# Performance work log

Hardware: AMD Instinct MI355X
Metric: run time of the kernel (lower is better)

The kernel has to match this reference:

```python
import jax, jax.numpy as jnp
import numpy as np

B, S, H2 = 32, 4096, 512  # H2 = 2*hidden_size


def setup_inputs() -> dict:
    key = jax.random.key(0)
    ks = jax.random.split(key, 10)
    s = 1.0 / np.sqrt(H2)
    return {
        "decoder_state": jax.random.normal(ks[0], (B, 1, H2), jnp.float32),
        "encoder_outputs": jax.random.normal(ks[1], (B, S, H2), jnp.float32),
        "coverage_vector": jax.random.uniform(ks[2], (B, S, H2), jnp.float32),
        "W_h": jax.random.uniform(ks[3], (H2, H2), jnp.float32, -s, s),
        "b_h": jax.random.uniform(ks[4], (H2,), jnp.float32, -s, s),
        "W_s": jax.random.uniform(ks[5], (H2, H2), jnp.float32, -s, s),
        "b_s": jax.random.uniform(ks[6], (H2,), jnp.float32, -s, s),
        "W_c": jax.random.uniform(ks[7], (H2, H2), jnp.float32, -s, s),
        "b_c": jax.random.uniform(ks[8], (H2,), jnp.float32, -s, s),
        "v": jax.random.uniform(ks[9], (H2, 1), jnp.float32, -s, s),
    }


def reference(decoder_state, encoder_outputs, coverage_vector,
              W_h, b_h, W_s, b_s, W_c, b_c, v):
    # additive attention features: [B, S, 2H]
    e = jnp.tanh(encoder_outputs @ W_h + b_h
                 + decoder_state @ W_s + b_s      # broadcasts over S
                 + coverage_vector @ W_c + b_c)
    scores = e @ v                                # [B, S, 1]
    attn_dist = jax.nn.softmax(scores, axis=1)    # softmax over source positions
    # weighted sum of encoder outputs: [B, 1, 2H]
    h_star_t = jnp.einsum('bsi,bsd->bid', attn_dist, encoder_outputs)
    coverage_new = coverage_vector + attn_dist    # broadcast over feature dim
    return h_star_t, attn_dist, coverage_new
```

## Files before the change

### kernel.cpp

```cpp
#include <hip/hip_runtime.h>
#include <hip/hip_bf16.h>
#include <stdint.h>

#define H2    512
#define BATCH 32
#define SEQ   4096
#define BM    64
#define NKT   32

typedef __attribute__((ext_vector_type(4))) float f32x4;
typedef __attribute__((ext_vector_type(8))) short bf16x8;

__device__ __forceinline__ unsigned short f2bf(float f) {
    union { float f; unsigned u; } v; v.f = f;
    unsigned r = v.u + 0x7FFF + ((v.u >> 16) & 1);
    return (unsigned short)(r >> 16);
}

__device__ __forceinline__ uint2 cvt4_bf16(f32x4 a) {
    uint2 r;
    asm("v_cvt_pk_bf16_f32 %0, %1, %2" : "=v"(r.x) : "v"(a[0]), "v"(a[1]));
    asm("v_cvt_pk_bf16_f32 %0, %1, %2" : "=v"(r.y) : "v"(a[2]), "v"(a[3]));
    return r;
}

__device__ __forceinline__ float fast_tanh(float x) {
    float e = __builtin_amdgcn_exp2f(x * 2.88539008177793f);
    return 1.0f - 2.0f * __builtin_amdgcn_rcpf(e + 1.0f);
}

__global__ void kzero(float* __restrict__ p) {
    int i = blockIdx.x * blockDim.x + threadIdx.x;
    if (i < 16416) p[i] = 0.0f;
}

__global__ void kprep_w(const float* __restrict__ Wh, const float* __restrict__ Wc,
                        unsigned short* __restrict__ wt) {
    int c    = blockIdx.x * blockDim.x + threadIdx.x;
    int lane = c & 63;
    int cb   = (c >> 6) & 31;
    int kt   = c >> 11;
    int col  = cb * 16 + (lane & 15);
    int k0   = kt * 32 + (lane >> 4) * 8;
    unsigned short tmp[8];
#pragma unroll
    for (int j = 0; j < 8; ++j) {
        int kg = k0 + j;
        float w = (kg < 512) ? Wh[kg * 512 + col] : Wc[(kg - 512) * 512 + col];
        tmp[j] = f2bf(w);
    }
    *reinterpret_cast<uint4*>(wt + (size_t)c * 8) = *reinterpret_cast<const uint4*>(tmp);
}

__global__ void kprep_q(const float* __restrict__ dec, const float* __restrict__ Ws,
                        const float* __restrict__ bh, const float* __restrict__ bs,
                        const float* __restrict__ bc, float* __restrict__ q) {
    __shared__ float dsh[512];
    int b = blockIdx.x, t = threadIdx.x;
    dsh[t]       = dec[b * 512 + t];
    dsh[t + 256] = dec[b * 512 + 256 + t];
    __syncthreads();
    float a0 = 0.f, a1 = 0.f;
#pragma unroll 4
    for (int k = 0; k < 512; ++k) {
        float d = dsh[k];
        a0 = fmaf(d, Ws[k * 512 + t], a0);
        a1 = fmaf(d, Ws[k * 512 + 256 + t], a1);
    }
    q[b * 512 + t]       = a0 + bh[t] + bs[t] + bc[t];
    q[b * 512 + 256 + t] = a1 + bh[256 + t] + bs[256 + t] + bc[256 + t];
}

__launch_bounds__(512, 4)
__global__ void kgemm(const float* __restrict__ enc, const float* __restrict__ cov,
                      const unsigned short* __restrict__ wt,
                      const float* __restrict__ q, const float* __restrict__ vvec,
                      float* __restrict__ wout, float* __restrict__ hun,
                      float* __restrict__ Zb) {
    __shared__ unsigned short Asm[3][2048];
    __shared__ float qv[H2];
    __shared__ float vv[H2];
    __shared__ float sred[BM][8];
    __shared__ float wsh[BM];

    int tid  = threadIdx.x;
    int lane = tid & 63, wn = tid >> 6;

    int cpx  = gridDim.x >> 3;
    int swz  = (blockIdx.x & 7) * cpx + (blockIdx.x >> 3);
    int row0 = swz * BM;
    int b    = row0 >> 12;

    qv[tid] = q[b * H2 + tid];
    vv[tid] = vvec[tid];

    int r = tid >> 3, k4 = tid & 7;
    const float* aeb = enc + (size_t)(row0 + r) * H2 + k4 * 4;
    const float* acb = cov + (size_t)(row0 + r) * H2 + k4 * 4;
    unsigned awb = (unsigned)((r >> 4) * 1024 + (k4 >> 1) * 256 +
                              (((r & 15) * 16) ^ ((k4 >> 1) << 4)) + (k4 & 1) * 8);
    unsigned arb = (unsigned)((lane >> 4) * 256 +
                              (((lane & 15) * 16) ^ ((lane >> 4) << 4)));
    const bf16x8* bb = reinterpret_cast<const bf16x8*>(wt) +
                       (size_t)(wn * 4) * 64 + lane;

    f32x4  acc[4][4] = {};
    bf16x8 af[4], bfr[4];
    f32x4  pa;

#define A_SRC(T) (((T) < 16) ? (aeb + (T) * 32) : (acb + ((T) - 16) * 32))
#define SB0 __builtin_amdgcn_sched_barrier(0);

    pa = *reinterpret_cast<const f32x4*>(A_SRC(0));
#pragma unroll
    for (int ni = 0; ni < 4; ++ni) bfr[ni] = bb[ni * 64];
    SB0
    { uint2 u = cvt4_bf16(pa);
      *reinterpret_cast<uint2*>((char*)Asm[0] + awb) = u; }
    pa = *reinterpret_cast<const f32x4*>(A_SRC(1));
    SB0
    { uint2 u = cvt4_bf16(pa);
      *reinterpret_cast<uint2*>((char*)Asm[1] + awb) = u; }
    pa = *reinterpret_cast<const f32x4*>(A_SRC(2));
    asm volatile("s_waitcnt lgkmcnt(0)" ::: "memory");
    SB0
    __builtin_amdgcn_s_barrier();
    SB0
#pragma unroll
    for (int mi = 0; mi < 4; ++mi)
        af[mi] = *reinterpret_cast<const bf16x8*>((char*)Asm[0] + mi * 1024 + arb);

    unsigned ro = 4096, wo = 8192;

#pragma unroll 1
    for (int t = 0; t < NKT; ++t) {
        __builtin_amdgcn_s_setprio(1);
#pragma unroll
        for (int mi = 0; mi < 4; ++mi)
#pragma unroll
            for (int ni = 0; ni < 4; ++ni)
                acc[mi][ni] = __builtin_amdgcn_mfma_f32_16x16x32_bf16(
                    af[mi], bfr[ni], acc[mi][ni], 0, 0, 0);
        __builtin_amdgcn_s_setprio(0);
        SB0
        if (t < NKT - 1) {
#pragma unroll
            for (int mi = 0; mi < 4; ++mi)
                af[mi] = *reinterpret_cast<const bf16x8*>(
                    (char*)Asm[0] + ro + mi * 1024 + arb);
            SB0
#pragma unroll
            for (int ni = 0; ni < 4; ++ni)
                bfr[ni] = bb[(size_t)(t + 1) * 2048 + ni * 64];
            SB0
        }
        if (t < NKT - 2) {
            uint2 u = cvt4_bf16(pa);
            *reinterpret_cast<uint2*>((char*)Asm[0] + wo + awb) = u;
        }
        if (t < NKT - 3) {
            pa = *reinterpret_cast<const f32x4*>(A_SRC(t + 3));
        }
        asm volatile("s_waitcnt lgkmcnt(0)" ::: "memory");
        SB0
        __builtin_amdgcn_s_barrier();
        SB0
        ro = (ro == 8192) ? 0u : ro + 4096;
        wo = (wo == 8192) ? 0u : wo + 4096;
    }
#undef A_SRC
#undef SB0

    float ps[4][4] = {};
#pragma unroll
    for (int mi = 0; mi < 4; ++mi)
#pragma unroll
        for (int ni = 0; ni < 4; ++ni) {
            int colg = wn * 64 + ni * 16 + (lane & 15);
            float qq = qv[colg], vl = vv[colg];
#pragma unroll
            for (int j = 0; j < 4; ++j) {
                float e = fast_tanh(acc[mi][ni][j] + qq);
                ps[mi][j] = fmaf(e, vl, ps[mi][j]);
            }
        }
#pragma unroll
    for (int mi = 0; mi < 4; ++mi)
#pragma unroll
        for (int j = 0; j < 4; ++j) {
            float s = ps[mi][j];
            s += __shfl_xor(s, 1);
            s += __shfl_xor(s, 2);
            s += __shfl_xor(s, 4);
            s += __shfl_xor(s, 8);
            if ((lane & 15) == 0)
                sred[mi * 16 + (lane >> 4) * 4 + j][wn] = s;
        }
    __syncthreads();

    if (tid < BM) {
        float s = 0.f;
#pragma unroll
        for (int w = 0; w < 8; ++w) s += sred[tid][w];
        float wv = __builtin_amdgcn_exp2f((s - 16.0f) * 1.4426950408889634f);
        wsh[tid] = wv;
        wout[row0 + tid] = wv;
        float zs = wv;
#pragma unroll
        for (int o = 1; o < 64; o <<= 1) zs += __shfl_xor(zs, o);
        if (tid == 0) atomicAdd(&Zb[b], zs);
    }
    __syncthreads();

    float hacc = 0.f;
#pragma unroll 8
    for (int rr = 0; rr < BM; ++rr)
        hacc = fmaf(wsh[rr], enc[(size_t)(row0 + rr) * H2 + tid], hacc);
    atomicAdd(&hun[b * H2 + tid], hacc);
}

__global__ void knorm(const float* __restrict__ hun, const float* __restrict__ Zb,
                      float* __restrict__ out) {
    int i = blockIdx.x * blockDim.x + threadIdx.x;
    int b = i >> 9;
    out[i] = hun[i] / Zb[b];
}

__global__ void kcov2(const float* __restrict__ cov, const float* __restrict__ w,
                      const float* __restrict__ Zb, float* __restrict__ out) {
    float* attn = out + 16384;
    float* covn = out + 16384 + 131072;
    int blk = blockIdx.x;
    int b = blk >> 6, ck = blk & 63;
    int s0 = ck * 64;
    int t  = threadIdx.x;
    int f4 = (t & 127) * 4;
    int rp = t >> 7;
    float rZ = 1.0f / Zb[b];
    size_t base = (size_t)b * SEQ * H2;
#pragma unroll 2
    for (int i = 0; i < 32; ++i) {
        int s = s0 + i * 2 + rp;
        float a = w[b * 4096 + s] * rZ;
        size_t idx = base + (size_t)s * H2 + f4;
        f32x4 c4 = *reinterpret_cast<const f32x4*>(cov + idx);
        c4 += a;
        __builtin_nontemporal_store(c4, reinterpret_cast<f32x4*>(covn + idx));
        if (f4 == 0) attn[b * 4096 + s] = a;
    }
}

extern "C" void kernel_launch(void* const* d_in, const int* in_sizes, int n_in,
                              void* d_out, int out_size, void* d_ws, size_t ws_size,
                              hipStream_t stream) {
    const float* dec = (const float*)d_in[0];
    const float* enc = (const float*)d_in[1];
    const float* cov = (const float*)d_in[2];
    const float* Wh  = (const float*)d_in[3];
    const float* bh  = (const float*)d_in[4];
    const float* Ws  = (const float*)d_in[5];
    const float* bs  = (const float*)d_in[6];
    const float* Wc  = (const float*)d_in[7];
    const float* bc  = (const float*)d_in[8];
    const float* v   = (const float*)d_in[9];
    float* out = (float*)d_out;

    char* ws = (char*)d_ws;
    unsigned short* wt = (unsigned short*)ws;
    float* q    = (float*)(ws + 0x100000);
    float* wbuf = (float*)(ws + 0x110000);
    float* hun  = (float*)(ws + 0x190000);
    float* Zb   = (float*)(ws + 0x1A0000);

    kzero   <<<dim3(65),   dim3(256),  0, stream>>>(hun);
    kprep_w <<<dim3(256),  dim3(256),  0, stream>>>(Wh, Wc, wt);
    kprep_q <<<dim3(32),   dim3(256),  0, stream>>>(dec, Ws, bh, bs, bc, q);
    kgemm   <<<dim3(2048), dim3(512),  0, stream>>>(enc, cov, wt, q, v,
                                                    wbuf, hun, Zb);
    knorm   <<<dim3(64),   dim3(256),  0, stream>>>(hun, Zb, out);
    kcov2   <<<dim3(2048), dim3(256),  0, stream>>>(cov, wbuf, Zb, out);
}
```

Baseline: 386.0 us.

## Use K=64 double-buffered A staging and replace atomics with partial reductions

The GEMM main loop now stages 64-wide K chunks (8 floats per thread, 16-byte LDS writes) into a two-buffer LDS ring and runs two MFMA groups per barrier, which halves the number of barriers and widens the global loads. Atomic accumulation of the context vector and normaliser is replaced by per-block partial buffers that a reworked knorm kernel reduces, and the zeroing kernel is removed. The weighted-sum loop uses four accumulators. The cost is extra workspace traffic for the partials (about 4MB) and a serial 64-element reduction inside knorm.

```diff
diff --git a/kernel.cpp b/kernel.cpp
--- a/kernel.cpp
+++ b/kernel.cpp
@@ -6,7 +6,7 @@
 #define BATCH 32
 #define SEQ   4096
 #define BM    64
-#define NKT   32
+#define NPER  16
 
 typedef __attribute__((ext_vector_type(4))) float f32x4;
 typedef __attribute__((ext_vector_type(8))) short bf16x8;
@@ -17,21 +17,18 @@
     return (unsigned short)(r >> 16);
 }
 
-__device__ __forceinline__ uint2 cvt4_bf16(f32x4 a) {
-    uint2 r;
-    asm("v_cvt_pk_bf16_f32 %0, %1, %2" : "=v"(r.x) : "v"(a[0]), "v"(a[1]));
-    asm("v_cvt_pk_bf16_f32 %0, %1, %2" : "=v"(r.y) : "v"(a[2]), "v"(a[3]));
+__device__ __forceinline__ uint4 cvt8_bf16(f32x4 lo, f32x4 hi) {
+    uint4 r;
+    asm("v_cvt_pk_bf16_f32 %0, %1, %2" : "=v"(r.x) : "v"(lo[0]), "v"(lo[1]));
+    asm("v_cvt_pk_bf16_f32 %0, %1, %2" : "=v"(r.y) : "v"(lo[2]), "v"(lo[3]));
+    asm("v_cvt_pk_bf16_f32 %0, %1, %2" : "=v"(r.z) : "v"(hi[0]), "v"(hi[1]));
+    asm("v_cvt_pk_bf16_f32 %0, %1, %2" : "=v"(r.w) : "v"(hi[2]), "v"(hi[3]));
     return r;
 }
 
 __device__ __forceinline__ float fast_tanh(float x) {
     float e = __builtin_amdgcn_exp2f(x * 2.88539008177793f);
     return 1.0f - 2.0f * __builtin_amdgcn_rcpf(e + 1.0f);
-}
-
-__global__ void kzero(float* __restrict__ p) {
-    int i = blockIdx.x * blockDim.x + threadIdx.x;
-    if (i < 16416) p[i] = 0.0f;
 }
 
 __global__ void kprep_w(const float* __restrict__ Wh, const float* __restrict__ Wc,
@@ -75,9 +72,9 @@
 __global__ void kgemm(const float* __restrict__ enc, const float* __restrict__ cov,
                       const unsigned short* __restrict__ wt,
                       const float* __restrict__ q, const float* __restrict__ vvec,
-                      float* __restrict__ wout, float* __restrict__ hun,
-                      float* __restrict__ Zb) {
-    __shared__ unsigned short Asm[3][2048];
+                      float* __restrict__ wout, float* __restrict__ hpart,
+                      float* __restrict__ Zpart) {
+    __shared__ unsigned short Asm[2][4096];
     __shared__ float qv[H2];
     __shared__ float vv[H2];
     __shared__ float sred[BM][8];
@@ -94,82 +91,98 @@
     qv[tid] = q[b * H2 + tid];
     vv[tid] = vvec[tid];
 
-    int r = tid >> 3, k4 = tid & 7;
-    const float* aeb = enc + (size_t)(row0 + r) * H2 + k4 * 4;
-    const float* acb = cov + (size_t)(row0 + r) * H2 + k4 * 4;
-    unsigned awb = (unsigned)((r >> 4) * 1024 + (k4 >> 1) * 256 +
-                              (((r & 15) * 16) ^ ((k4 >> 1) << 4)) + (k4 & 1) * 8);
+    int r = tid >> 3, k8 = tid & 7;
+    const float* aeb = enc + (size_t)(row0 + r) * H2 + k8 * 8;
+    const float* acb = cov + (size_t)(row0 + r) * H2 + k8 * 8;
+    unsigned awb = (unsigned)((k8 >> 2) * 4096 + (r >> 4) * 1024 + (k8 & 3) * 256 +
+                              (((r & 15) * 16) ^ ((k8 & 3) << 4)));
     unsigned arb = (unsigned)((lane >> 4) * 256 +
                               (((lane & 15) * 16) ^ ((lane >> 4) << 4)));
     const bf16x8* bb = reinterpret_cast<const bf16x8*>(wt) +
                        (size_t)(wn * 4) * 64 + lane;
 
     f32x4  acc[4][4] = {};
-    bf16x8 af[4], bfr[4];
-    f32x4  pa;
-
-#define A_SRC(T) (((T) < 16) ? (aeb + (T) * 32) : (acb + ((T) - 16) * 32))
+    bf16x8 bfr[4], af[4];
+    f32x4  pA[2][2];
+
 #define SB0 __builtin_amdgcn_sched_barrier(0);
-
-    pa = *reinterpret_cast<const f32x4*>(A_SRC(0));
-#pragma unroll
-    for (int ni = 0; ni < 4; ++ni) bfr[ni] = bb[ni * 64];
-    SB0
-    { uint2 u = cvt4_bf16(pa);
-      *reinterpret_cast<uint2*>((char*)Asm[0] + awb) = u; }
-    pa = *reinterpret_cast<const f32x4*>(A_SRC(1));
-    SB0
-    { uint2 u = cvt4_bf16(pa);
-      *reinterpret_cast<uint2*>((char*)Asm[1] + awb) = u; }
-    pa = *reinterpret_cast<const f32x4*>(A_SRC(2));
+#define A_PTR(T) ((((T) < 8) ? aeb : acb) + ((T) & 7) * 64)
+#define DS_AF(CUR, S)                                                          \
+    _Pragma("unroll")                                                          \
+    for (int mi = 0; mi < 4; ++mi)                                             \
+        af[mi] = *reinterpret_cast<const bf16x8*>(                             \
+            (char*)Asm[CUR] + (S) * 4096 + mi * 1024 + arb);
+#define LOAD_B(KT32)                                                           \
+    _Pragma("unroll")                                                          \
+    for (int ni = 0; ni < 4; ++ni)                                             \
+        bfr[ni] = bb[(size_t)(KT32) * 2048 + ni * 64];
+#define MFMA16                                                                 \
+    __builtin_amdgcn_s_setprio(1);                                             \
+    _Pragma("unroll")                                                          \
+    for (int mi = 0; mi < 4; ++mi)                                             \
+        _Pragma("unroll")                                                      \
+        for (int ni = 0; ni < 4; ++ni)                                         \
+            acc[mi][ni] = __builtin_amdgcn_mfma_f32_16x16x32_bf16(             \
+                af[mi], bfr[ni], acc[mi][ni], 0, 0, 0);                        \
+    __builtin_amdgcn_s_setprio(0);
+
+#define BODY(T, CUR, PC, DO_PN, DO_B0, DO_STAGE)                               \
+  {                                                                            \
+    DS_AF(CUR, 0)                                                              \
+    SB0                                                                        \
+    MFMA16                                  \
+    SB0                                                                        \
+    LOAD_B((T) * 2 + 1)                            \
+    DS_AF(CUR, 1)                                                              \
+    if (DO_PN) {                                                               \
+        const float* _p = A_PTR((T) + 2);                                      \
+        pA[(PC) ^ 1][0] = *reinterpret_cast<const f32x4*>(_p);                 \
+        pA[(PC) ^ 1][1] = *reinterpret_cast<const f32x4*>(_p + 4);             \
+    }                                                                          \
+    SB0                                                                        \
+    MFMA16                   \
+    SB0                                                                        \
+    if (DO_B0) { LOAD_B((T) * 2 + 2) }          \
+    if (DO_STAGE) {                                                            \
+        uint4 _u = cvt8_bf16(pA[PC][0], pA[PC][1]);                            \
+        *reinterpret_cast<uint4*>((char*)Asm[(CUR) ^ 1] + awb) = _u;           \
+    }                                                                          \
+    asm volatile("s_waitcnt lgkmcnt(0)" ::: "memory");                         \
+    SB0                                                                        \
+    __builtin_amdgcn_s_barrier();                                              \
+    SB0                                                                        \
+  }
+
+    LOAD_B(0)
+    {
+        f32x4 a0 = *reinterpret_cast<const f32x4*>(aeb);
+        f32x4 a1 = *reinterpret_cast<const f32x4*>(aeb + 4);
+        pA[1][0] = *reinterpret_cast<const f32x4*>(aeb + 64);
+        pA[1][1] = *reinterpret_cast<const f32x4*>(aeb + 68);
+        SB0
+        uint4 u = cvt8_bf16(a0, a1);
+        *reinterpret_cast<uint4*>((char*)Asm[0] + awb) = u;
+    }
     asm volatile("s_waitcnt lgkmcnt(0)" ::: "memory");
     SB0
     __builtin_amdgcn_s_barrier();
     SB0
-#pragma unroll
-    for (int mi = 0; mi < 4; ++mi)
-        af[mi] = *reinterpret_cast<const bf16x8*>((char*)Asm[0] + mi * 1024 + arb);
-
-    unsigned ro = 4096, wo = 8192;
 
 #pragma unroll 1
-    for (int t = 0; t < NKT; ++t) {
-        __builtin_amdgcn_s_setprio(1);
-#pragma unroll
-        for (int mi = 0; mi < 4; ++mi)
-#pragma unroll
-            for (int ni = 0; ni < 4; ++ni)
-                acc[mi][ni] = __builtin_amdgcn_mfma_f32_16x16x32_bf16(
-                    af[mi], bfr[ni], acc[mi][ni], 0, 0, 0);
-        __builtin_amdgcn_s_setprio(0);
-        SB0
-        if (t < NKT - 1) {
-#pragma unroll
-            for (int mi = 0; mi < 4; ++mi)
-                af[mi] = *reinterpret_cast<const bf16x8*>(
-                    (char*)Asm[0] + ro + mi * 1024 + arb);
-            SB0
-#pragma unroll
-            for (int ni = 0; ni < 4; ++ni)
-                bfr[ni] = bb[(size_t)(t + 1) * 2048 + ni * 64];
-            SB0
-        }
-        if (t < NKT - 2) {
-            uint2 u = cvt4_bf16(pa);
-            *reinterpret_cast<uint2*>((char*)Asm[0] + wo + awb) = u;
-        }
-        if (t < NKT - 3) {
-            pa = *reinterpret_cast<const f32x4*>(A_SRC(t + 3));
-        }
-        asm volatile("s_waitcnt lgkmcnt(0)" ::: "memory");
-        SB0
-        __builtin_amdgcn_s_barrier();
-        SB0
-        ro = (ro == 8192) ? 0u : ro + 4096;
-        wo = (wo == 8192) ? 0u : wo + 4096;
-    }
-#undef A_SRC
+    for (int p = 0; p < 7; ++p) {
+        const int t0 = p * 2;
+        BODY(t0,     0, 1, true, true, true)
+        BODY(t0 + 1, 1, 0, true, true, true)
+    }
+    BODY(14, 0, 1, false, true,  true)
+    BODY(15, 1, 0, false, false, false)
+
 #undef SB0
+#undef A_PTR
+#undef DS_AF
+#undef LOAD_B
+#undef MFMA16
+#undef BODY
 
     float ps[4][4] = {};
 #pragma unroll
@@ -208,22 +221,41 @@
         float zs = wv;
 #pragma unroll
         for (int o = 1; o < 64; o <<= 1) zs += __shfl_xor(zs, o);
-        if (tid == 0) atomicAdd(&Zb[b], zs);
+        if (tid == 0) Zpart[swz] = zs;
     }
     __syncthreads();
 
-    float hacc = 0.f;
+    {
+        const float* eb = enc + (size_t)row0 * H2 + tid;
+        float h0 = 0.f, h1 = 0.f, h2 = 0.f, h3 = 0.f;
+#pragma unroll 4
+        for (int rr = 0; rr < BM; rr += 4) {
+            h0 = fmaf(wsh[rr + 0], eb[(size_t)(rr + 0) * H2], h0);
+            h1 = fmaf(wsh[rr + 1], eb[(size_t)(rr + 1) * H2], h1);
+            h2 = fmaf(wsh[rr + 2], eb[(size_t)(rr + 2) * H2], h2);
+            h3 = fmaf(wsh[rr + 3], eb[(size_t)(rr + 3) * H2], h3);
+        }
+        hpart[(size_t)swz * H2 + tid] = (h0 + h1) + (h2 + h3);
+    }
+}
+
+__global__ void knorm(const float* __restrict__ hpart, const float* __restrict__ Zpart,
+                      float* __restrict__ Zb, float* __restrict__ out) {
+    __shared__ float zsh;
+    int b = blockIdx.x, t = threadIdx.x;
+    if (t == 0) {
+        float z = 0.f;
 #pragma unroll 8
-    for (int rr = 0; rr < BM; ++rr)
-        hacc = fmaf(wsh[rr], enc[(size_t)(row0 + rr) * H2 + tid], hacc);
-    atomicAdd(&hun[b * H2 + tid], hacc);
-}
-
-__global__ void knorm(const float* __restrict__ hun, const float* __restrict__ Zb,
-                      float* __restrict__ out) {
-    int i = blockIdx.x * blockDim.x + threadIdx.x;
-    int b = i >> 9;
-    out[i] = hun[i] / Zb[b];
+        for (int i = 0; i < 64; ++i) z += Zpart[b * 64 + i];
+        zsh = z;
+        Zb[b] = z;
+    }
+    float h = 0.f;
+    const float* hp = hpart + (size_t)b * 64 * H2 + t;
+#pragma unroll 8
+    for (int i = 0; i < 64; ++i) h += hp[(size_t)i * H2];
+    __syncthreads();
+    out[b * H2 + t] = h / zsh;
 }
 
 __global__ void kcov2(const float* __restrict__ cov, const float* __restrict__ w,
@@ -267,16 +299,16 @@
 
     char* ws = (char*)d_ws;
     unsigned short* wt = (unsigned short*)ws;
-    float* q    = (float*)(ws + 0x100000);
-    float* wbuf = (float*)(ws + 0x110000);
-    float* hun  = (float*)(ws + 0x190000);
-    float* Zb   = (float*)(ws + 0x1A0000);
-
-    kzero   <<<dim3(65),   dim3(256),  0, stream>>>(hun);
+    float* q     = (float*)(ws + 0x100000);
+    float* wbuf  = (float*)(ws + 0x110000);
+    float* hpart = (float*)(ws + 0x190000);
+    float* Zpart = (float*)(ws + 0x590000);
+    float* Zb    = (float*)(ws + 0x592000);
+
     kprep_w <<<dim3(256),  dim3(256),  0, stream>>>(Wh, Wc, wt);
     kprep_q <<<dim3(32),   dim3(256),  0, stream>>>(dec, Ws, bh, bs, bc, q);
     kgemm   <<<dim3(2048), dim3(512),  0, stream>>>(enc, cov, wt, q, v,
-                                                    wbuf, hun, Zb);
-    knorm   <<<dim3(64),   dim3(256),  0, stream>>>(hun, Zb, out);
+                                                    wbuf, hpart, Zpart);
+    knorm   <<<dim3(32),   dim3(512),  0, stream>>>(hpart, Zpart, Zb, out);
     kcov2   <<<dim3(2048), dim3(256),  0, stream>>>(cov, wbuf, Zb, out);
 }
```

Result: faster. 367.7 us (median of 3 runs) (-4.8%).
